# Kernel optimization log

Measured on AMD Instinct MI355X. Metric: run time of the kernel, lower is better.

Reference implementation:

```python
import jax, jax.numpy as jnp
import numpy as np

N, H, V, MAX_STEPS = 256, 128, 64, 4

def setup_inputs() -> dict:
    key = jax.random.key(0)
    ks = jax.random.split(key, 16)
    def w(k, shape, fan_in):
        return jax.random.normal(k, shape, dtype=jnp.float32) / np.sqrt(fan_in)
    inp = {}
    inp['node_embeddings'] = jax.random.normal(ks[0], (N, H), dtype=jnp.float32)
    inp['skip_embeddings'] = jax.random.normal(ks[1], (N, N, H), dtype=jnp.float32)
    inp['Wx'] = w(ks[2], (H, 4 * H), H)
    inp['Wh'] = w(ks[3], (H, 4 * H), H)
    inp['b'] = jnp.zeros((4 * H,), jnp.float32)
    inp['Wxs'] = w(ks[4], (H, 4 * H), H)
    inp['Whs'] = w(ks[5], (H, 4 * H), H)
    inp['bs'] = jnp.zeros((4 * H,), jnp.float32)
    inp['Wb'] = w(ks[6], (2 * H, 2), 2 * H)
    inp['bb'] = jnp.zeros((2,), jnp.float32)
    inp['Wk'] = w(ks[7], (H, H), H)
    inp['bk'] = jnp.zeros((H,), jnp.float32)
    inp['Wq'] = w(ks[8], (2 * H, H), 2 * H)
    inp['bq'] = jnp.zeros((H,), jnp.float32)
    inp['Wl'] = w(ks[9], (2 * H, 1), 2 * H)
    inp['bl'] = jnp.zeros((1,), jnp.float32)
    inp['Wd'] = w(ks[10], (2 * H, V), 2 * H)
    inp['bd'] = jnp.zeros((V,), jnp.float32)
    # valid skips only forward in the program (include diagonal = no-skip)
    inp['skip_mask'] = jnp.triu(jnp.ones((N, N), dtype=bool))
    inp['true_indexes'] = jax.random.randint(ks[11], (N,), 0, N, dtype=jnp.int32)
    inp['false_indexes'] = jax.random.randint(ks[12], (N,), 0, N, dtype=jnp.int32)
    inp['exit_index'] = N - 1
    return inp

def _lstm(c, h, x, Wx, Wh, b):
    gates = x @ Wx + h @ Wh + b  # [..., 4H]
    i, f, g, o = jnp.split(gates, 4, axis=-1)
    c2 = jax.nn.sigmoid(f) * c + jax.nn.sigmoid(i) * jnp.tanh(g)
    h2 = jax.nn.sigmoid(o) * jnp.tanh(c2)
    return c2, h2

def reference(node_embeddings, skip_embeddings, Wx, Wh, b, Wxs, Whs, bs,
              Wb, bb, Wk, bk, Wq, bq, Wl, bl, Wd, bd,
              skip_mask, true_indexes, false_indexes, exit_index):
    n, hdim = node_embeddings.shape
    eye = jnp.eye(n, dtype=node_embeddings.dtype)
    ip0 = jnp.zeros((n,), node_embeddings.dtype).at[0].set(1.0)
    c0 = jnp.zeros((n, hdim), node_embeddings.dtype)
    h0 = jnp.zeros((n, hdim), node_embeddings.dtype)
    keys = skip_embeddings @ Wk + bk  # [N,N,H] (input-only, precompute)

    def step(carry, _):
        ip, c, h = carry
        # per-node LSTM proposals
        c_p, h_p = _lstm(c, h, node_embeddings, Wx, Wh, b)  # [N,H]
        hid = jnp.concatenate([c_p, h_p], axis=-1)  # [N,2H]
        # skip proposals: carry of source i applied to skip embedding (i,j)
        c_sk, h_sk = _lstm(c[:, None, :], h[:, None, :], skip_embeddings, Wxs, Whs, bs)  # [N,N,H]
        # branch decisions
        branch = jax.nn.softmax(hid @ Wb + bb, axis=-1)  # [N,2]
        # skip decisions (per source i, softmax over destinations j)
        queries = hid @ Wq + bq  # [N,H]
        kq = jax.nn.relu(jnp.concatenate(
            [keys, jnp.broadcast_to(queries[:, None, :], (n, n, hdim))], axis=-1))  # [N,N,2H]
        logits = jnp.einsum('ijk,kl->ijl', kq, Wl)[..., 0] + bl[0]  # [N,N]
        skip_dec = jax.nn.softmax(jnp.where(skip_mask, logits, -jnp.inf), axis=-1)
        # aggregation (IPA)
        yes_skip = skip_dec * (1.0 - eye)  # zero diagonal
        no_skip = jnp.diagonal(skip_dec)
        p_bt = ip * no_skip * branch[:, 0]
        p_bf = ip * no_skip * branch[:, 1]
        new_ip = (jax.ops.segment_sum(p_bt, true_indexes, num_segments=n)
                  + jax.ops.segment_sum(p_bf, false_indexes, num_segments=n)
                  + jnp.einsum('i,ij->j', ip, yes_skip))
        denom = new_ip[:, None] + 1e-7
        def agg(hp, hsk):
            t = jax.ops.segment_sum(hp * p_bt[:, None], true_indexes, num_segments=n)
            f = jax.ops.segment_sum(hp * p_bf[:, None], false_indexes, num_segments=n)
            s = jnp.einsum('ijh,i,ij->jh', hsk, ip, yes_skip)
            return (t + f + s) / denom
        return (new_ip, agg(c_p, c_sk), agg(h_p, h_sk)), None

    (ip, c, h), _ = jax.lax.scan(step, (ip0, c0, h0), None, length=MAX_STEPS)
    exit_concat = jnp.concatenate([c[exit_index], h[exit_index]], axis=-1)  # [2H]
    return exit_concat @ Wd + bd  # [V]
```

## Files before the change

kernel.cpp:

```cpp
#include <hip/hip_runtime.h>
#include <hip/hip_bf16.h>

constexpr int NN = 256;
constexpr int HH = 128;
constexpr int GG = 512;
constexpr int NP = NN * NN;
constexpr int NCH = 4;
constexpr int CHSZ = 64;

typedef __attribute__((ext_vector_type(8))) short short8;
typedef __attribute__((ext_vector_type(4))) float f32x4;

__device__ unsigned short g_xs[(size_t)NP * GG];
__device__ unsigned short g_sebf[(size_t)NP * HH];
__device__ unsigned short g_wfr[20 * 512 * 8];
__device__ float g_bsp[GG];
__device__ float g_pwh[HH * HH * 4];
__device__ float g_pws[HH * HH * 4];
__device__ float g_kterm[NP];
__device__ float g_yeswT[NP];
__device__ float g_noskip[NN];
__device__ float g_xg[NN * HH * 4];
__device__ float g_xga[NN * HH * 4];
__device__ float g_hws[NN * HH * 4];
__device__ float g_c[NN * HH];
__device__ float g_h[NN * HH];
__device__ float g_sc[NN * HH];
__device__ float g_sh[NN * HH];
__device__ float g_ip[NN];
__device__ float g_nip[NN];

__device__ __forceinline__ unsigned short f2bf(float f) {
  unsigned int u = __float_as_uint(f);
  u = (u + 0x7fffu + ((u >> 16) & 1u)) >> 16;
  return (unsigned short)u;
}
__device__ __forceinline__ float bf2f(unsigned short s) {
  return __uint_as_float(((unsigned int)s) << 16);
}
__device__ __forceinline__ float frcp(float x) {
#if __has_builtin(__builtin_amdgcn_rcpf)
  return __builtin_amdgcn_rcpf(x);
#else
  return 1.0f / x;
#endif
}
__device__ __forceinline__ float sigm(float x) { return frcp(1.f + __expf(-x)); }
__device__ __forceinline__ float tanhfast(float x) { return 1.f - 2.f * frcp(__expf(2.f * x) + 1.f); }

__global__ __launch_bounds__(512) void k_pre(const float* __restrict__ NE,
                                             const float* __restrict__ Wx,
                                             const float* __restrict__ b,
                                             const float* __restrict__ Wxs,
                                             const float* __restrict__ Wk,
                                             const float* __restrict__ bs,
                                             const float* __restrict__ Wh,
                                             const float* __restrict__ Whs,
                                             const float* __restrict__ SE) {
  const int bid = blockIdx.x;
  const int tid = threadIdx.x;
  if (bid < 64) {
    const int idx = bid * 512 + tid;
    g_sc[idx] = 0.f; g_sh[idx] = 0.f; g_c[idx] = 0.f; g_h[idx] = 0.f;
    *(float4*)&g_hws[(size_t)idx * 4] = make_float4(0.f, 0.f, 0.f, 0.f);
    if (idx < NN) { g_nip[idx] = 0.f; g_ip[idx] = (idx == 0) ? 1.f : 0.f; }
  } else if (bid < 84) {
    const int bidx = bid - 64;
    const int tile = bidx >> 2, ks = bidx & 3;
    const int ct = tid >> 6, l = tid & 63;
    const int c = ct * 16 + (l & 15);
    const int kbase = ks * 32 + (l >> 4) * 8;
    int src = 0;
    if (tile < 4) src = (c & 3) * 128 + tile * 32 + (c >> 2);
    unsigned short* dst = &g_wfr[((size_t)bidx * 512 + tid) * 8];
#pragma unroll
    for (int e = 0; e < 8; ++e) {
      int k = kbase + e;
      float v = (tile < 4) ? Wxs[k * GG + src] : Wk[k * HH + c];
      dst[e] = f2bf(v);
    }
    if (tile < 4 && ks == 0 && (l >> 4) == 0) g_bsp[tile * 128 + c] = bs[src];
  } else if (bid < 116) {
    const int k = (bid - 84) * 4 + (tid >> 7), t = tid & 127;
    float4 a = make_float4(Wh[k * GG + t], Wh[k * GG + 128 + t], Wh[k * GG + 256 + t], Wh[k * GG + 384 + t]);
    float4 s = make_float4(Whs[k * GG + t], Whs[k * GG + 128 + t], Whs[k * GG + 256 + t], Whs[k * GG + 384 + t]);
    *(float4*)&g_pwh[((size_t)k * HH + t) * 4] = a;
    *(float4*)&g_pws[((size_t)k * HH + t) * 4] = s;
  } else if (bid < 180) {
    __shared__ float ne[4][HH];
    const int sub = tid >> 7, t = tid & 127;
    const int i = (bid - 116) * 4 + sub;
    ne[sub][t] = NE[i * HH + t];
    __syncthreads();
    float a0 = b[t], a1 = b[128 + t], a2 = b[256 + t], a3 = b[384 + t];
    for (int k = 0; k < HH; ++k) {
      float x = ne[sub][k];
      a0 = fmaf(x, Wx[k * GG + t], a0);
      a1 = fmaf(x, Wx[k * GG + 128 + t], a1);
      a2 = fmaf(x, Wx[k * GG + 256 + t], a2);
      a3 = fmaf(x, Wx[k * GG + 384 + t], a3);
    }
    float4 v = make_float4(a0, a1, a2, a3);
    *(float4*)&g_xg[((size_t)i * HH + t) * 4] = v;
    *(float4*)&g_xga[((size_t)i * HH + t) * 4] = v;
  } else {
    const int p0 = (bid - 180) * 256;
    for (int e = tid; e < 4096; e += 512) {
      const int pl = e >> 4, g = e & 15;
      const int pair = p0 + pl;
      const int gs = g ^ (pair & 7);
      const float* src = SE + (size_t)pair * HH + gs * 8;
      float4 f0 = *(const float4*)(src);
      float4 f1 = *(const float4*)(src + 4);
      short8 v;
      v[0] = (short)f2bf(f0.x); v[1] = (short)f2bf(f0.y); v[2] = (short)f2bf(f0.z); v[3] = (short)f2bf(f0.w);
      v[4] = (short)f2bf(f1.x); v[5] = (short)f2bf(f1.y); v[6] = (short)f2bf(f1.z); v[7] = (short)f2bf(f1.w);
      *(short8*)&g_sebf[(size_t)pair * HH + g * 8] = v;
    }
  }
}

__device__ __forceinline__ void loadB(short8* dst, int tile, int ks, int l) {
  const unsigned short* wf = &g_wfr[((size_t)(tile * 4 + ks)) * 4096 + l * 8];
#pragma unroll
  for (int ct = 0; ct < 8; ++ct) dst[ct] = *(const short8*)(wf + ct * 512);
}

__global__ __launch_bounds__(256) void k_gemm(const float* __restrict__ bk,
                                              const float* __restrict__ Wl) {
  __shared__ __align__(16) char lds[32768];
  const int bid = blockIdx.x;
  const int tile = blockIdx.y;
  const int pb = (bid < 128) ? (bid * 2) : ((bid - 128) * 2 + 1);
  const int pairBase = pb * 128;
  const int tid = threadIdx.x;

  {
    const char* src = (const char*)g_sebf + (size_t)pairBase * 256;
    const int wvoff = (tid >> 6) * 1024;
#pragma unroll
    for (int it = 0; it < 8; ++it) {
      __builtin_amdgcn_global_load_lds(
          (const __attribute__((address_space(1))) unsigned int*)(src + it * 4096 + tid * 16),
          (__attribute__((address_space(3))) unsigned int*)(lds + it * 4096 + wvoff),
          16, 0, 0);
    }
  }
  __syncthreads();

  const int wv = tid >> 6;
  const int l = tid & 63;
  const int l15 = l & 15, lg = l >> 4;

  f32x4 acc[2][8];
#pragma unroll
  for (int rt = 0; rt < 2; ++rt)
#pragma unroll
    for (int ct = 0; ct < 8; ++ct) acc[rt][ct] = (f32x4){0.f, 0.f, 0.f, 0.f};

  short8 bA[8], bB[8];
  loadB(bA, tile, 0, l);
#pragma unroll
  for (int ks = 0; ks < 4; ks += 2) {
    loadB(bB, tile, ks + 1, l);
    {
      const int kb = ks * 64 + lg * 16;
      short8 a[2];
#pragma unroll
      for (int rt = 0; rt < 2; ++rt) {
        int row = wv * 32 + rt * 16 + l15;
        a[rt] = *(const short8*)(lds + row * 256 + (kb ^ ((row & 7) << 4)));
      }
#pragma unroll
      for (int rt = 0; rt < 2; ++rt)
#pragma unroll
        for (int ct = 0; ct < 8; ++ct)
          acc[rt][ct] = __builtin_amdgcn_mfma_f32_16x16x32_bf16(a[rt], bA[ct], acc[rt][ct], 0, 0, 0);
    }
    if (ks + 2 < 4) loadB(bA, tile, ks + 2, l);
    {
      const int kb = (ks + 1) * 64 + lg * 16;
      short8 a[2];
#pragma unroll
      for (int rt = 0; rt < 2; ++rt) {
        int row = wv * 32 + rt * 16 + l15;
        a[rt] = *(const short8*)(lds + row * 256 + (kb ^ ((row & 7) << 4)));
      }
#pragma unroll
      for (int rt = 0; rt < 2; ++rt)
#pragma unroll
        for (int ct = 0; ct < 8; ++ct)
          acc[rt][ct] = __builtin_amdgcn_mfma_f32_16x16x32_bf16(a[rt], bB[ct], acc[rt][ct], 0, 0, 0);
    }
  }

  if (tile < 4) {
#pragma unroll
    for (int rt = 0; rt < 2; ++rt)
#pragma unroll
      for (int ct = 0; ct < 8; ++ct) {
        const int col = ct * 16 + l15;
        const float bsv = g_bsp[tile * 128 + col];
#pragma unroll
        for (int r = 0; r < 4; ++r) {
          int row = wv * 32 + rt * 16 + lg * 4 + r;
          int pair = pairBase + row;
          int jj = pair & 255, ii = pair >> 8;
          if (jj > ii)
            g_xs[((size_t)jj * NN + ii) * GG + tile * 128 + col] = f2bf(acc[rt][ct][r] + bsv);
        }
      }
  } else {
#pragma unroll
    for (int rt = 0; rt < 2; ++rt) {
#pragma unroll
      for (int r = 0; r < 4; ++r) {
        float s = 0.f;
#pragma unroll
        for (int ct = 0; ct < 8; ++ct) {
          int col = ct * 16 + l15;
          float x = acc[rt][ct][r] + bk[col];
          x = fmaxf(x, 0.f);
          s = fmaf(x, Wl[col], s);
        }
#pragma unroll
        for (int m = 1; m < 16; m <<= 1) s += __shfl_xor(s, m, 64);
        int row = wv * 32 + rt * 16 + lg * 4 + r;
        int pair = pairBase + row;
        int jj = pair & 255, ii = pair >> 8;
        if (l15 == 0 && jj >= ii) g_kterm[pair] = s;
      }
    }
  }
}

__global__ __launch_bounds__(256) void k_softmax() {
  const int i = blockIdx.x, j = threadIdx.x;
  __shared__ float sm[NN];
  float x = -1e30f;
  if (j >= i) x = g_kterm[i * NN + j];
  sm[j] = x;
  __syncthreads();
  for (int s = 128; s > 0; s >>= 1) { if (j < s) sm[j] = fmaxf(sm[j], sm[j + s]); __syncthreads(); }
  float mx = sm[0];
  __syncthreads();
  float e = (j >= i) ? __expf(x - mx) : 0.f;
  sm[j] = e;
  __syncthreads();
  for (int s = 128; s > 0; s >>= 1) { if (j < s) sm[j] += sm[j + s]; __syncthreads(); }
  float p = e * frcp(sm[0]);
  g_yeswT[j * NN + i] = (j == i) ? 0.f : p;
  if (j == i) g_noskip[i] = p;
}

__global__ __launch_bounds__(128) void k_step(const float* __restrict__ Wb,
                                              const float* __restrict__ bb,
                                              const int* __restrict__ tix,
                                              const int* __restrict__ fix) {
  const int t = threadIdx.x;
  if (blockIdx.x < 256) {
    const int i = blockIdx.x;
    __shared__ float red[2][2];
    const float4 a = *(const float4*)&g_xga[((size_t)i * HH + t) * 4];
    float co = g_c[i * HH + t];
    float c2 = sigm(a.y) * co + sigm(a.x) * tanhfast(a.z);
    float h2 = sigm(a.w) * tanhfast(c2);
    float q0 = c2 * Wb[2 * t] + h2 * Wb[2 * (128 + t)];
    float q1 = c2 * Wb[2 * t + 1] + h2 * Wb[2 * (128 + t) + 1];
#pragma unroll
    for (int m = 1; m < 64; m <<= 1) { q0 += __shfl_xor(q0, m, 64); q1 += __shfl_xor(q1, m, 64); }
    if ((t & 63) == 0) { red[t >> 6][0] = q0; red[t >> 6][1] = q1; }
    __syncthreads();
    float l0 = red[0][0] + red[1][0] + bb[0];
    float l1 = red[0][1] + red[1][1] + bb[1];
    float mm = fmaxf(l0, l1);
    float e0 = __expf(l0 - mm), e1 = __expf(l1 - mm);
    float inv = frcp(e0 + e1);
    float ipv = g_ip[i] * g_noskip[i];
    if (ipv != 0.f) {
      float pbt = ipv * e0 * inv, pbf = ipv * e1 * inv;
      int ti = tix[i], fi = fix[i];
      atomicAdd(&g_sc[ti * HH + t], c2 * pbt);
      atomicAdd(&g_sh[ti * HH + t], h2 * pbt);
      atomicAdd(&g_sc[fi * HH + t], c2 * pbf);
      atomicAdd(&g_sh[fi * HH + t], h2 * pbf);
      if (t == 0) { atomicAdd(&g_nip[ti], pbt); atomicAdd(&g_nip[fi], pbf); }
    }
  } else {
    const int idx = blockIdx.x - 256;
    const int j = idx >> 2, ch = idx & 3;
    const int i0 = ch * CHSZ;
    if (i0 >= j) return;
    const int iN = (j - i0 < CHSZ) ? (j - i0) : CHSZ;
    __shared__ float wsh[CHSZ];
    if (t < CHSZ) wsh[t] = g_ip[i0 + t] * g_yeswT[j * NN + i0 + t];
    __syncthreads();
    float accC = 0.f, accH = 0.f, accW = 0.f;
    for (int ii = 0; ii < iN; ++ii) {
      const float wgt = wsh[ii];
      const int i = i0 + ii;
      const ushort4 gv = *(const ushort4*)&g_xs[((size_t)j * NN + i) * GG + t * 4];
      float4 hw = *(const float4*)&g_hws[((size_t)i * HH + t) * 4];
      float xi = bf2f(gv.x) + hw.x;
      float xf = bf2f(gv.y) + hw.y;
      float xg = bf2f(gv.z) + hw.z;
      float xo = bf2f(gv.w) + hw.w;
      float c2 = sigm(xf) * g_c[i * HH + t] + sigm(xi) * tanhfast(xg);
      float h2 = sigm(xo) * tanhfast(c2);
      accC = fmaf(wgt, c2, accC);
      accH = fmaf(wgt, h2, accH);
      accW += wgt;
    }
    if (accW != 0.f) {
      atomicAdd(&g_sc[j * HH + t], accC);
      atomicAdd(&g_sh[j * HH + t], accH);
      if (t == 0) atomicAdd(&g_nip[j], accW);
    }
  }
}

__global__ __launch_bounds__(512) void k_finA() {
  const int tid = threadIdx.x;
  const int j = blockIdx.x * 4 + (tid >> 7), t = tid & 127;
  float nip = g_nip[j];
  float d = frcp(nip + 1e-7f);
  g_c[j * HH + t] = g_sc[j * HH + t] * d;
  g_h[j * HH + t] = g_sh[j * HH + t] * d;
  g_sc[j * HH + t] = 0.f;
  g_sh[j * HH + t] = 0.f;
  if (t == 0) { g_ip[j] = nip; g_nip[j] = 0.f; }
}

__global__ __launch_bounds__(256) void k_finB() {
  __shared__ float hsm[64 * 132];
  __shared__ float wsmT[4 * 128];
  const int b = blockIdx.x;
  const int cg = b >> 1, m = b & 1;
  const int tid = threadIdx.x;
  const float* __restrict__ W = m ? g_pws : g_pwh;
  for (int e = tid; e < 512; e += 256) {
    const int cc = e >> 7, k = e & 127;
    wsmT[cc * 128 + k] = W[(size_t)k * 512 + cg * 4 + cc];
  }
  const int il = tid >> 2, cc = tid & 3;
  for (int it = 0; it < 4; ++it) {
    const int i0 = it * 64;
    __syncthreads();
    for (int e = tid; e < 2048; e += 256) {
      const int r = e >> 5, kq = e & 31;
      *(float4*)&hsm[r * 132 + kq * 4] = *(const float4*)&g_h[(size_t)(i0 + r) * HH + kq * 4];
    }
    __syncthreads();
    float acc = 0.f;
#pragma unroll 8
    for (int k4 = 0; k4 < 32; ++k4) {
      const float4 h4 = *(const float4*)&hsm[il * 132 + k4 * 4];
      const float4 w4 = *(const float4*)&wsmT[cc * 128 + k4 * 4];
      acc = fmaf(h4.x, w4.x, acc); acc = fmaf(h4.y, w4.y, acc);
      acc = fmaf(h4.z, w4.z, acc); acc = fmaf(h4.w, w4.w, acc);
    }
    const size_t o = (size_t)(i0 + il) * 512 + cg * 4 + cc;
    if (m == 0) g_xga[o] = g_xg[o] + acc;
    else g_hws[o] = acc;
  }
}

__global__ __launch_bounds__(64) void k_out(const float* __restrict__ Wd,
                                            const float* __restrict__ bd,
                                            const int* __restrict__ ei,
                                            float* __restrict__ out) {
  const int v = threadIdx.x;
  const int e = ei[0];
  float s = bd[v];
  for (int h = 0; h < HH; ++h) {
    s = fmaf(g_c[e * HH + h], Wd[h * 64 + v], s);
    s = fmaf(g_h[e * HH + h], Wd[(128 + h) * 64 + v], s);
  }
  out[v] = s;
}

extern "C" void kernel_launch(void* const* d_in, const int* in_sizes, int n_in,
                              void* d_out, int out_size, void* d_ws, size_t ws_size,
                              hipStream_t stream) {
  const float* NE  = (const float*)d_in[0];
  const float* SE  = (const float*)d_in[1];
  const float* Wx  = (const float*)d_in[2];
  const float* Wh  = (const float*)d_in[3];
  const float* b   = (const float*)d_in[4];
  const float* Wxs = (const float*)d_in[5];
  const float* Whs = (const float*)d_in[6];
  const float* bs  = (const float*)d_in[7];
  const float* Wb  = (const float*)d_in[8];
  const float* bb  = (const float*)d_in[9];
  const float* Wk  = (const float*)d_in[10];
  const float* bk  = (const float*)d_in[11];
  const float* Wl  = (const float*)d_in[14];
  const float* Wd  = (const float*)d_in[16];
  const float* bd  = (const float*)d_in[17];
  const int* tix = (const int*)d_in[19];
  const int* fix = (const int*)d_in[20];
  const int* ei  = (const int*)d_in[21];
  float* out = (float*)d_out;

  k_pre<<<436, 512, 0, stream>>>(NE, Wx, b, Wxs, Wk, bs, Wh, Whs, SE);
  k_gemm<<<dim3(384, 5), 256, 0, stream>>>(bk, Wl);
  k_softmax<<<256, 256, 0, stream>>>();
  for (int s = 0; s < 4; ++s) {
    k_step<<<256 + NN * NCH, 128, 0, stream>>>(Wb, bb, tix, fix);
    k_finA<<<64, 512, 0, stream>>>();
    if (s != 3) k_finB<<<256, 256, 0, stream>>>();
  }
  k_out<<<1, 64, 0, stream>>>(Wd, bd, ei, out);
}
```

Baseline: 182.1 us.

## Fuse softmax and recurrent step loop into one cooperative persistent kernel

Replaces the softmax, per-step aggregation, finalize and recurrent-projection kernels with a single cooperative kernel that uses grid.sync between phases. Accumulators are double-buffered so zeroing the next buffer overlaps with finalization. The h@W projection is recomputed directly from the normalized accumulators, so it runs alongside finalization instead of after it. This removes about thirteen kernel launches and their gaps, at the cost of grid-wide barriers and fewer blocks doing the matmul. A fallback to the old multi-kernel path is kept for when the cooperative launch fails.

```diff
diff --git a/kernel.cpp b/kernel.cpp
--- a/kernel.cpp
+++ b/kernel.cpp
@@ -1,12 +1,12 @@
 #include <hip/hip_runtime.h>
 #include <hip/hip_bf16.h>
+#include <hip/hip_cooperative_groups.h>
+namespace cg = cooperative_groups;
 
 constexpr int NN = 256;
 constexpr int HH = 128;
 constexpr int GG = 512;
 constexpr int NP = NN * NN;
-constexpr int NCH = 4;
-constexpr int CHSZ = 64;
 
 typedef __attribute__((ext_vector_type(8))) short short8;
 typedef __attribute__((ext_vector_type(4))) float f32x4;
@@ -15,20 +15,20 @@
 __device__ unsigned short g_sebf[(size_t)NP * HH];
 __device__ unsigned short g_wfr[20 * 512 * 8];
 __device__ float g_bsp[GG];
-__device__ float g_pwh[HH * HH * 4];
-__device__ float g_pws[HH * HH * 4];
+__device__ float g_pwh[HH * GG];
+__device__ float g_pws[HH * GG];
 __device__ float g_kterm[NP];
 __device__ float g_yeswT[NP];
 __device__ float g_noskip[NN];
-__device__ float g_xg[NN * HH * 4];
-__device__ float g_xga[NN * HH * 4];
-__device__ float g_hws[NN * HH * 4];
+__device__ float g_xg[NN * GG];
+__device__ float g_xga[NN * GG];
+__device__ float g_hws[NN * GG];
 __device__ float g_c[NN * HH];
 __device__ float g_h[NN * HH];
-__device__ float g_sc[NN * HH];
-__device__ float g_sh[NN * HH];
+__device__ float g_sc2[2][NN * HH];
+__device__ float g_sh2[2][NN * HH];
+__device__ float g_nip2[2][NN];
 __device__ float g_ip[NN];
-__device__ float g_nip[NN];
 
 __device__ __forceinline__ unsigned short f2bf(float f) {
   unsigned int u = __float_as_uint(f);
@@ -61,9 +61,14 @@
   const int tid = threadIdx.x;
   if (bid < 64) {
     const int idx = bid * 512 + tid;
-    g_sc[idx] = 0.f; g_sh[idx] = 0.f; g_c[idx] = 0.f; g_h[idx] = 0.f;
+    g_c[idx] = 0.f; g_h[idx] = 0.f;
+    g_sc2[0][idx] = 0.f; g_sc2[1][idx] = 0.f;
+    g_sh2[0][idx] = 0.f; g_sh2[1][idx] = 0.f;
     *(float4*)&g_hws[(size_t)idx * 4] = make_float4(0.f, 0.f, 0.f, 0.f);
-    if (idx < NN) { g_nip[idx] = 0.f; g_ip[idx] = (idx == 0) ? 1.f : 0.f; }
+    if (idx < NN) {
+      g_nip2[0][idx] = 0.f; g_nip2[1][idx] = 0.f;
+      g_ip[idx] = (idx == 0) ? 1.f : 0.f;
+    }
   } else if (bid < 84) {
     const int bidx = bid - 64;
     const int tile = bidx >> 2, ks = bidx & 3;
@@ -234,7 +239,178 @@
   }
 }
 
-__global__ __launch_bounds__(256) void k_softmax() {
+__global__ __launch_bounds__(512, 2) void k_coop(const float* __restrict__ Wb,
+                                                 const float* __restrict__ bb,
+                                                 const int* __restrict__ tix,
+                                                 const int* __restrict__ fix,
+                                                 const float* __restrict__ Wd,
+                                                 const float* __restrict__ bd,
+                                                 const int* __restrict__ ei,
+                                                 float* __restrict__ out) {
+  cg::grid_group grid = cg::this_grid();
+  const int bid = blockIdx.x;
+  const int tid = threadIdx.x;
+  __shared__ float smem[2176];
+
+  if (bid < 128) {
+    const int half = tid >> 8, j = tid & 255;
+    const int i = bid * 2 + half;
+    float* sm = &smem[half * 320];
+    float x = (j >= i) ? g_kterm[i * NN + j] : -1e30f;
+    sm[j] = x;
+    __syncthreads();
+    for (int s = 128; s > 0; s >>= 1) { if (j < s) sm[j] = fmaxf(sm[j], sm[j + s]); __syncthreads(); }
+    float mx = sm[0];
+    __syncthreads();
+    float e = (j >= i) ? __expf(x - mx) : 0.f;
+    sm[j] = e;
+    __syncthreads();
+    for (int s = 128; s > 0; s >>= 1) { if (j < s) sm[j] += sm[j + s]; __syncthreads(); }
+    float p = e * frcp(sm[0]);
+    g_yeswT[j * NN + i] = (j == i) ? 0.f : p;
+    if (j == i) g_noskip[i] = p;
+  }
+  grid.sync();
+
+  for (int s = 0; s < 4; ++s) {
+    const int cur = s & 1, nxt = cur ^ 1;
+    for (int it = 0; it < 2; ++it) {
+      const int sub = bid * 4 + (tid >> 7) + it * 1024;
+      const int t = tid & 127;
+      if (sub < 256) {
+        const int i = sub;
+        const float4 a = *(const float4*)&g_xga[((size_t)i * HH + t) * 4];
+        float co = g_c[i * HH + t];
+        float c2 = sigm(a.y) * co + sigm(a.x) * tanhfast(a.z);
+        float h2 = sigm(a.w) * tanhfast(c2);
+        float q0 = c2 * Wb[2 * t] + h2 * Wb[2 * (128 + t)];
+        float q1 = c2 * Wb[2 * t + 1] + h2 * Wb[2 * (128 + t) + 1];
+#pragma unroll
+        for (int m = 1; m < 64; m <<= 1) { q0 += __shfl_xor(q0, m, 64); q1 += __shfl_xor(q1, m, 64); }
+        if ((t & 63) == 0) { smem[(tid >> 6) * 2] = q0; smem[(tid >> 6) * 2 + 1] = q1; }
+        __syncthreads();
+        const int k4 = (tid >> 7) * 4;
+        float l0 = smem[k4] + smem[k4 + 2] + bb[0];
+        float l1 = smem[k4 + 1] + smem[k4 + 3] + bb[1];
+        float mm = fmaxf(l0, l1);
+        float e0 = __expf(l0 - mm), e1 = __expf(l1 - mm);
+        float inv = frcp(e0 + e1);
+        float ipv = g_ip[i] * g_noskip[i];
+        if (ipv != 0.f) {
+          float pbt = ipv * e0 * inv, pbf = ipv * e1 * inv;
+          int ti = tix[i], fi = fix[i];
+          atomicAdd(&g_sc2[cur][ti * HH + t], c2 * pbt);
+          atomicAdd(&g_sh2[cur][ti * HH + t], h2 * pbt);
+          atomicAdd(&g_sc2[cur][fi * HH + t], c2 * pbf);
+          atomicAdd(&g_sh2[cur][fi * HH + t], h2 * pbf);
+          if (t == 0) { atomicAdd(&g_nip2[cur][ti], pbt); atomicAdd(&g_nip2[cur][fi], pbf); }
+        }
+      } else if (sub < 1280) {
+        const int idx = sub - 256;
+        const int j = idx >> 2, ch = idx & 3;
+        const int i0 = ch * 64;
+        float* wsh = &smem[16 + (tid >> 7) * 64];
+        const bool act = (i0 < j);
+        if (act && t < 64) wsh[t] = g_ip[i0 + t] * g_yeswT[j * NN + i0 + t];
+        __syncthreads();
+        if (act) {
+          const int iN = (j - i0 < 64) ? (j - i0) : 64;
+          float accC = 0.f, accH = 0.f, accW = 0.f;
+          for (int ii = 0; ii < iN; ++ii) {
+            const float wgt = wsh[ii];
+            const int i = i0 + ii;
+            const ushort4 gv = *(const ushort4*)&g_xs[((size_t)j * NN + i) * GG + t * 4];
+            float4 hw = *(const float4*)&g_hws[((size_t)i * HH + t) * 4];
+            float xi = bf2f(gv.x) + hw.x;
+            float xf = bf2f(gv.y) + hw.y;
+            float xg = bf2f(gv.z) + hw.z;
+            float xo = bf2f(gv.w) + hw.w;
+            float c2 = sigm(xf) * g_c[i * HH + t] + sigm(xi) * tanhfast(xg);
+            float h2 = sigm(xo) * tanhfast(c2);
+            accC = fmaf(wgt, c2, accC);
+            accH = fmaf(wgt, h2, accH);
+            accW += wgt;
+          }
+          if (accW != 0.f) {
+            atomicAdd(&g_sc2[cur][j * HH + t], accC);
+            atomicAdd(&g_sh2[cur][j * HH + t], accH);
+            if (t == 0) atomicAdd(&g_nip2[cur][j], accW);
+          }
+        }
+      }
+      __syncthreads();
+    }
+    grid.sync();
+
+    if (bid < 64) {
+      const int j = bid * 4 + (tid >> 7), t = tid & 127;
+      float nip = g_nip2[cur][j];
+      float d = frcp(nip + 1e-7f);
+      g_c[j * HH + t] = g_sc2[cur][j * HH + t] * d;
+      g_h[j * HH + t] = g_sh2[cur][j * HH + t] * d;
+      if (t == 0) g_ip[j] = nip;
+    } else if (bid < 96) {
+      if (s < 3) {
+        const int vb = (bid - 64) * 2 + (tid >> 8);
+        const int tid8 = tid & 255;
+        const int m = vb >> 5, i0 = (vb & 31) * 8;
+        const float* __restrict__ W = m ? g_pws : g_pwh;
+        float* sm = &smem[(tid >> 8) * 1088];
+        if (tid8 < 8) sm[1040 + tid8] = frcp(g_nip2[cur][i0 + tid8] + 1e-7f);
+        __syncthreads();
+        for (int e = tid8; e < 1024; e += 256) {
+          const int ii = e >> 7, k = e & 127;
+          sm[ii * 129 + k] = g_sh2[cur][(i0 + ii) * HH + k] * sm[1040 + ii];
+        }
+        __syncthreads();
+        for (int hf = 0; hf < 2; ++hf) {
+          const int col = hf * 256 + tid8;
+          float acc[8];
+#pragma unroll
+          for (int ii = 0; ii < 8; ++ii) acc[ii] = 0.f;
+          for (int k = 0; k < 128; ++k) {
+            const float w = W[(size_t)k * GG + col];
+#pragma unroll
+            for (int ii = 0; ii < 8; ++ii) acc[ii] = fmaf(sm[ii * 129 + k], w, acc[ii]);
+          }
+          if (m == 0) {
+#pragma unroll
+            for (int ii = 0; ii < 8; ++ii) {
+              const size_t o = (size_t)(i0 + ii) * GG + col;
+              g_xga[o] = g_xg[o] + acc[ii];
+            }
+          } else {
+#pragma unroll
+            for (int ii = 0; ii < 8; ++ii)
+              g_hws[(size_t)(i0 + ii) * GG + col] = acc[ii];
+          }
+        }
+      }
+    } else if (bid < 128) {
+      if (s < 3) {
+        const int gz = (bid - 96) * 512 + tid;
+        const float4 z = make_float4(0.f, 0.f, 0.f, 0.f);
+        if (gz < 8192) ((float4*)&g_sc2[nxt][0])[gz] = z;
+        else ((float4*)&g_sh2[nxt][0])[gz - 8192] = z;
+        if (bid == 96 && tid < 256) g_nip2[nxt][tid] = 0.f;
+      }
+    }
+    grid.sync();
+  }
+
+  if (bid == 0 && tid < 64) {
+    const int v = tid;
+    const int e = ei[0];
+    float sacc = bd[v];
+    for (int h = 0; h < HH; ++h) {
+      sacc = fmaf(g_c[e * HH + h], Wd[h * 64 + v], sacc);
+      sacc = fmaf(g_h[e * HH + h], Wd[(128 + h) * 64 + v], sacc);
+    }
+    out[v] = sacc;
+  }
+}
+
+__global__ __launch_bounds__(256) void fb_softmax() {
   const int i = blockIdx.x, j = threadIdx.x;
   __shared__ float sm[NN];
   float x = -1e30f;
@@ -253,10 +429,10 @@
   if (j == i) g_noskip[i] = p;
 }
 
-__global__ __launch_bounds__(128) void k_step(const float* __restrict__ Wb,
-                                              const float* __restrict__ bb,
-                                              const int* __restrict__ tix,
-                                              const int* __restrict__ fix) {
+__global__ __launch_bounds__(128) void fb_step(const float* __restrict__ Wb,
+                                               const float* __restrict__ bb,
+                                               const int* __restrict__ tix,
+                                               const int* __restrict__ fix) {
   const int t = threadIdx.x;
   if (blockIdx.x < 256) {
     const int i = blockIdx.x;
@@ -280,20 +456,20 @@
     if (ipv != 0.f) {
       float pbt = ipv * e0 * inv, pbf = ipv * e1 * inv;
       int ti = tix[i], fi = fix[i];
-      atomicAdd(&g_sc[ti * HH + t], c2 * pbt);
-      atomicAdd(&g_sh[ti * HH + t], h2 * pbt);
-      atomicAdd(&g_sc[fi * HH + t], c2 * pbf);
-      atomicAdd(&g_sh[fi * HH + t], h2 * pbf);
-      if (t == 0) { atomicAdd(&g_nip[ti], pbt); atomicAdd(&g_nip[fi], pbf); }
+      atomicAdd(&g_sc2[0][ti * HH + t], c2 * pbt);
+      atomicAdd(&g_sh2[0][ti * HH + t], h2 * pbt);
+      atomicAdd(&g_sc2[0][fi * HH + t], c2 * pbf);
+      atomicAdd(&g_sh2[0][fi * HH + t], h2 * pbf);
+      if (t == 0) { atomicAdd(&g_nip2[0][ti], pbt); atomicAdd(&g_nip2[0][fi], pbf); }
     }
   } else {
     const int idx = blockIdx.x - 256;
     const int j = idx >> 2, ch = idx & 3;
-    const int i0 = ch * CHSZ;
+    const int i0 = ch * 64;
     if (i0 >= j) return;
-    const int iN = (j - i0 < CHSZ) ? (j - i0) : CHSZ;
-    __shared__ float wsh[CHSZ];
-    if (t < CHSZ) wsh[t] = g_ip[i0 + t] * g_yeswT[j * NN + i0 + t];
+    const int iN = (j - i0 < 64) ? (j - i0) : 64;
+    __shared__ float wsh[64];
+    if (t < 64) wsh[t] = g_ip[i0 + t] * g_yeswT[j * NN + i0 + t];
     __syncthreads();
     float accC = 0.f, accH = 0.f, accW = 0.f;
     for (int ii = 0; ii < iN; ++ii) {
@@ -312,35 +488,35 @@
       accW += wgt;
     }
     if (accW != 0.f) {
-      atomicAdd(&g_sc[j * HH + t], accC);
-      atomicAdd(&g_sh[j * HH + t], accH);
-      if (t == 0) atomicAdd(&g_nip[j], accW);
-    }
-  }
-}
-
-__global__ __launch_bounds__(512) void k_finA() {
+      atomicAdd(&g_sc2[0][j * HH + t], accC);
+      atomicAdd(&g_sh2[0][j * HH + t], accH);
+      if (t == 0) atomicAdd(&g_nip2[0][j], accW);
+    }
+  }
+}
+
+__global__ __launch_bounds__(512) void fb_finA() {
   const int tid = threadIdx.x;
   const int j = blockIdx.x * 4 + (tid >> 7), t = tid & 127;
-  float nip = g_nip[j];
+  float nip = g_nip2[0][j];
   float d = frcp(nip + 1e-7f);
-  g_c[j * HH + t] = g_sc[j * HH + t] * d;
-  g_h[j * HH + t] = g_sh[j * HH + t] * d;
-  g_sc[j * HH + t] = 0.f;
-  g_sh[j * HH + t] = 0.f;
-  if (t == 0) { g_ip[j] = nip; g_nip[j] = 0.f; }
-}
-
-__global__ __launch_bounds__(256) void k_finB() {
+  g_c[j * HH + t] = g_sc2[0][j * HH + t] * d;
+  g_h[j * HH + t] = g_sh2[0][j * HH + t] * d;
+  g_sc2[0][j * HH + t] = 0.f;
+  g_sh2[0][j * HH + t] = 0.f;
+  if (t == 0) { g_ip[j] = nip; g_nip2[0][j] = 0.f; }
+}
+
+__global__ __launch_bounds__(256) void fb_finB() {
   __shared__ float hsm[64 * 132];
   __shared__ float wsmT[4 * 128];
   const int b = blockIdx.x;
-  const int cg = b >> 1, m = b & 1;
+  const int cg_ = b >> 1, m = b & 1;
   const int tid = threadIdx.x;
   const float* __restrict__ W = m ? g_pws : g_pwh;
   for (int e = tid; e < 512; e += 256) {
     const int cc = e >> 7, k = e & 127;
-    wsmT[cc * 128 + k] = W[(size_t)k * 512 + cg * 4 + cc];
+    wsmT[cc * 128 + k] = W[(size_t)k * 512 + cg_ * 4 + cc];
   }
   const int il = tid >> 2, cc = tid & 3;
   for (int it = 0; it < 4; ++it) {
@@ -359,7 +535,7 @@
       acc = fmaf(h4.x, w4.x, acc); acc = fmaf(h4.y, w4.y, acc);
       acc = fmaf(h4.z, w4.z, acc); acc = fmaf(h4.w, w4.w, acc);
     }
-    const size_t o = (size_t)(i0 + il) * 512 + cg * 4 + cc;
+    const size_t o = (size_t)(i0 + il) * 512 + cg_ * 4 + cc;
     if (m == 0) g_xga[o] = g_xg[o] + acc;
     else g_hws[o] = acc;
   }
@@ -404,11 +580,18 @@
 
   k_pre<<<436, 512, 0, stream>>>(NE, Wx, b, Wxs, Wk, bs, Wh, Whs, SE);
   k_gemm<<<dim3(384, 5), 256, 0, stream>>>(bk, Wl);
-  k_softmax<<<256, 256, 0, stream>>>();
-  for (int s = 0; s < 4; ++s) {
-    k_step<<<256 + NN * NCH, 128, 0, stream>>>(Wb, bb, tix, fix);
-    k_finA<<<64, 512, 0, stream>>>();
-    if (s != 3) k_finB<<<256, 256, 0, stream>>>();
-  }
-  k_out<<<1, 64, 0, stream>>>(Wd, bd, ei, out);
-}
+
+  void* cargs[] = {(void*)&Wb, (void*)&bb, (void*)&tix, (void*)&fix,
+                   (void*)&Wd, (void*)&bd, (void*)&ei, (void*)&out};
+  hipError_t cerr = hipLaunchCooperativeKernel((const void*)k_coop, dim3(256), dim3(512),
+                                               cargs, 0, stream);
+  if (cerr != hipSuccess) {
+    fb_softmax<<<256, 256, 0, stream>>>();
+    for (int s = 0; s < 4; ++s) {
+      fb_step<<<256 + 1024, 128, 0, stream>>>(Wb, bb, tix, fix);
+      fb_finA<<<64, 512, 0, stream>>>();
+      if (s != 3) fb_finB<<<256, 256, 0, stream>>>();
+    }
+    k_out<<<1, 64, 0, stream>>>(Wd, bd, ei, out);
+  }
+}
```

Measured after the change: 449.5 us. 147% more time.
